# Optimization experiments

Measured on AMD Instinct MI355X. Metric: run time of the kernel, lower is better.

Reference implementation:

```python
import jax, jax.numpy as jnp
import numpy as np

N = 50000      # nodes
E = 800000     # edges (self-loop-free; reference appends self loops like PyG GATv2Conv)
IN = 128; H = 4; C = 64; HC = H * C; HID = 64; OUT = 2


def _gat_conv(x, wl, bl, wr, br, att, bias, src, dst, n):
    # PyG GATv2Conv: e_ij = att . leaky_relu(W_l x_j + W_r x_i); segment softmax over dst;
    # out_i = sum_j alpha_ij * (W_l x_j), heads concatenated, plus bias.
    xl = (x @ wl + bl).reshape(n, H, C)
    xr = (x @ wr + br).reshape(n, H, C)
    e = jnp.sum(att * jax.nn.leaky_relu(xl[src] + xr[dst], 0.2), axis=-1)  # [E+n, H]
    m = jax.ops.segment_max(e, dst, num_segments=n)                         # [n, H]
    ex = jnp.exp(e - m[dst])
    s = jax.ops.segment_sum(ex, dst, num_segments=n)
    alpha = ex / (s[dst] + 1e-16)
    out = jax.ops.segment_sum(xl[src] * alpha[..., None], dst, num_segments=n)
    return out.reshape(n, HC) + bias


def _graph_norm(x, w, b, ms, eps=1e-5):
    # PyG GraphNorm, single graph: normalize over all nodes
    mean = jnp.mean(x, axis=0)
    xc = x - ms * mean
    var = jnp.mean(xc * xc, axis=0)
    return w * xc / jnp.sqrt(var + eps) + b


def setup_inputs() -> dict:
    key = jax.random.key(0)
    k = jax.random.split(key, 16)
    x = jax.random.normal(k[0], (N, IN), dtype=jnp.float32)
    src = jax.random.randint(k[1], (E,), 0, N, dtype=jnp.int32)
    dst = jax.random.randint(k[2], (E,), 0, N, dtype=jnp.int32)
    dst = jnp.where(dst == src, (dst + 1) % N, dst)  # no self loops in raw edges
    edge_index = jnp.stack([src, dst])

    def lin(kk, fi, fo):
        return (jax.random.normal(kk, (fi, fo), jnp.float32) / np.float32(np.sqrt(fi)))

    zeros = lambda d: jnp.zeros((d,), jnp.float32)
    ones = lambda d: jnp.ones((d,), jnp.float32)
    return dict(
        x=x, edge_index=edge_index,
        conv0_wl=lin(k[3], IN, HC), conv0_bl=zeros(HC),
        conv0_wr=lin(k[4], IN, HC), conv0_br=zeros(HC),
        conv0_att=jax.random.normal(k[5], (H, C), jnp.float32) / np.float32(np.sqrt(C)),
        conv0_bias=zeros(HC),
        conv1_wl=lin(k[6], HC, HC), conv1_bl=zeros(HC),
        conv1_wr=lin(k[7], HC, HC), conv1_br=zeros(HC),
        conv1_att=jax.random.normal(k[8], (H, C), jnp.float32) / np.float32(np.sqrt(C)),
        conv1_bias=zeros(HC),
        gn0_w=ones(HC), gn0_b=zeros(HC), gn0_ms=ones(HC),
        gn1_w=ones(HC), gn1_b=zeros(HC), gn1_ms=ones(HC),
        lin0_w=lin(k[9], HC, HID), lin0_b=zeros(HID),
        lin1_w=lin(k[10], HID, HID), lin1_b=zeros(HID),
        lin2_w=lin(k[11], HID, OUT), lin2_b=zeros(OUT),
    )


def reference(x, edge_index, conv0_wl, conv0_bl, conv0_wr, conv0_br, conv0_att, conv0_bias,
              conv1_wl, conv1_bl, conv1_wr, conv1_br, conv1_att, conv1_bias,
              gn0_w, gn0_b, gn0_ms, gn1_w, gn1_b, gn1_ms,
              lin0_w, lin0_b, lin1_w, lin1_b, lin2_w, lin2_b):
    n = x.shape[0]
    loop = jnp.arange(n, dtype=edge_index.dtype)
    src = jnp.concatenate([edge_index[0], loop])  # add self loops (PyG default)
    dst = jnp.concatenate([edge_index[1], loop])
    # NOTE: original forward zips convs (3) with norms (2) -> only 2 convs execute.
    h = _gat_conv(x, conv0_wl, conv0_bl, conv0_wr, conv0_br, conv0_att, conv0_bias, src, dst, n)
    h = jax.nn.relu(_graph_norm(h, gn0_w, gn0_b, gn0_ms))
    h = _gat_conv(h, conv1_wl, conv1_bl, conv1_wr, conv1_br, conv1_att, conv1_bias, src, dst, n)
    h = jax.nn.relu(_graph_norm(h, gn1_w, gn1_b, gn1_ms))
    h = jax.nn.relu(h @ lin0_w + lin0_b)  # dropout_rate=None -> no dropout
    h = jax.nn.relu(h @ lin1_w + lin1_b)
    return h @ lin2_w + lin2_b
```

## Files before the change

kernel.cpp:

```cpp
#include <hip/hip_runtime.h>
#include <hip/hip_bf16.h>


typedef __bf16 bf16x8 __attribute__((ext_vector_type(8)));
typedef float  f32x4  __attribute__((ext_vector_type(4)));

__device__ __forceinline__ unsigned short f2b(float f) {
    unsigned u = __float_as_uint(f);
    return (unsigned short)((u + 0x7fffu + ((u >> 16) & 1u)) >> 16);
}

__device__ __forceinline__ unsigned pk_norm(unsigned u, float a0, float a1,
                                            float c0, float c1) {
    float lo = __uint_as_float(u << 16);
    float hi = __uint_as_float(u & 0xffff0000u);
    lo = fmaxf(fmaf(a0, lo, c0), 0.f);
    hi = fmaxf(fmaf(a1, hi, c1), 0.f);
    unsigned r;
    asm volatile("v_cvt_pk_bf16_f32 %0, %1, %2" : "=v"(r) : "v"(lo), "v"(hi));
    return r;
}

__device__ __forceinline__ void gload_lds16(const unsigned short* g, unsigned short* l) {
    __builtin_amdgcn_global_load_lds(
        (const __attribute__((address_space(1))) unsigned int*)g,
        (__attribute__((address_space(3))) unsigned int*)l, 16, 0, 0);
}

__global__ __launch_bounds__(256) void prep_all(
    const float* __restrict__ x, unsigned short* __restrict__ xbf, int nx4,
    const float* __restrict__ w0l, const float* __restrict__ w0r, unsigned short* __restrict__ Wt0,
    const float* __restrict__ w1l, const float* __restrict__ w1r, unsigned short* __restrict__ Wt1,
    const float* __restrict__ l0, unsigned short* __restrict__ Lt0,
    const float* __restrict__ l1, unsigned short* __restrict__ Lt1,
    float* __restrict__ zf, int* __restrict__ hist, int nh)
{
    int t = blockIdx.x * 256 + threadIdx.x;
    if (t < 512) { zf[t] = 0.f; }
    int i = t - 512;
    if (i >= 0 && i < nh) hist[i] = 0;
    i -= nh;
    if (i >= 0 && i < nx4) {
        float4 v = ((const float4*)x)[i];
        ushort4 o = { f2b(v.x), f2b(v.y), f2b(v.z), f2b(v.w) };
        ((ushort4*)xbf)[i] = o;
    }
    i -= nx4;
    if (i >= 0 && i < 32768) { int nn = i >> 7, kk = i & 127; Wt0[i] = f2b(w0l[kk * 256 + nn]); }
    i -= 32768;
    if (i >= 0 && i < 32768) { int nn = i >> 7, kk = i & 127; Wt0[32768 + i] = f2b(w0r[kk * 256 + nn]); }
    i -= 32768;
    if (i >= 0 && i < 65536) { int nn = i >> 8, kk = i & 255; Wt1[i] = f2b(w1l[kk * 256 + nn]); }
    i -= 65536;
    if (i >= 0 && i < 65536) { int nn = i >> 8, kk = i & 255; Wt1[65536 + i] = f2b(w1r[kk * 256 + nn]); }
    i -= 65536;
    if (i >= 0 && i < 16384) { int nn = i >> 8, kk = i & 255; Lt0[i] = f2b(l0[kk * 64 + nn]); }
    i -= 16384;
    if (i >= 0 && i < 4096)  { int nn = i >> 6, kk = i & 63;  Lt1[i] = f2b(l1[kk * 64 + nn]); }
}

template<int K, bool NORM>
__global__ __launch_bounds__(256) void conv_gemm(
    const unsigned short* __restrict__ A, const unsigned short* __restrict__ Bt,
    const float* __restrict__ bias0, const float* __restrict__ bias1, int split,
    const float* __restrict__ na, const float* __restrict__ nc,
    unsigned short* __restrict__ C, int M, int N, int nt)
{
    __shared__ unsigned short smem[128 * 136];
    unsigned short* sA = smem;
    unsigned short* sB = smem + 4096;

    const int nwg = gridDim.x;
    const int bid = blockIdx.x;
    const int q = nwg >> 3, r = nwg & 7;
    const int xcd = bid & 7, pos = bid >> 3;
    const int wgid = (xcd < r ? xcd * (q + 1) : r * (q + 1) + (xcd - r) * q) + pos;
    const int tm = wgid / nt;
    const int tn = wgid - tm * nt;

    const int lane = threadIdx.x & 63;
    const int w = threadIdx.x >> 6;
    const int wm = w >> 1, wn = w & 1;
    const int bm = tm * 128;
    const int bn = tn * 128;
    const int lr = lane & 15;
    const int g  = lane >> 4;

    const int srow = lane >> 2;
    const int sk   = ((lane & 3) ^ (srow & 3)) << 3;
    const int aslot = (g ^ (lr & 3)) << 3;

    f32x4 acc[4][4] = {};

    for (int k0 = 0; k0 < K; k0 += 32) {
        #pragma unroll
        for (int j = 0; j < 2; ++j) {
            const int row = w * 32 + j * 16 + srow;
            int ga = bm + row; if (ga >= M) ga = M - 1;
            gload_lds16(A + (size_t)ga * K + k0 + sk, sA + (size_t)(w * 32 + j * 16) * 32);
            gload_lds16(Bt + (size_t)(bn + row) * K + k0 + sk, sB + (size_t)(w * 32 + j * 16) * 32);
        }
        __syncthreads();

        bf16x8 afr[4], bfr[4];
        #pragma unroll
        for (int mi = 0; mi < 4; ++mi) {
            const int row = wm * 64 + mi * 16 + lr;
            afr[mi] = *(const bf16x8*)(sA + row * 32 + aslot);
        }
        #pragma unroll
        for (int ni = 0; ni < 4; ++ni) {
            const int row = wn * 64 + ni * 16 + lr;
            bfr[ni] = *(const bf16x8*)(sB + row * 32 + aslot);
        }
        if constexpr (NORM) {
            const int lk = g * 8;
            const float4 av0 = *(const float4*)(na + k0 + lk);
            const float4 av1 = *(const float4*)(na + k0 + lk + 4);
            const float4 cv0 = *(const float4*)(nc + k0 + lk);
            const float4 cv1 = *(const float4*)(nc + k0 + lk + 4);
            #pragma unroll
            for (int mi = 0; mi < 4; ++mi) {
                uint4 u = __builtin_bit_cast(uint4, afr[mi]);
                uint4 rr;
                rr.x = pk_norm(u.x, av0.x, av0.y, cv0.x, cv0.y);
                rr.y = pk_norm(u.y, av0.z, av0.w, cv0.z, cv0.w);
                rr.z = pk_norm(u.z, av1.x, av1.y, cv1.x, cv1.y);
                rr.w = pk_norm(u.w, av1.z, av1.w, cv1.z, cv1.w);
                afr[mi] = __builtin_bit_cast(bf16x8, rr);
            }
        }
        #pragma unroll
        for (int mi = 0; mi < 4; ++mi)
            #pragma unroll
            for (int ni = 0; ni < 4; ++ni)
                acc[mi][ni] = __builtin_amdgcn_mfma_f32_16x16x32_bf16(
                    bfr[ni], afr[mi], acc[mi][ni], 0, 0, 0);
        __syncthreads();
    }

    unsigned short (*cs)[136] = (unsigned short(*)[136])smem;
    #pragma unroll
    for (int ni = 0; ni < 4; ++ni) {
        const int lcol = wn * 64 + ni * 16 + g * 4;
        const int col = bn + lcol;
        const float4 bv = (col < split)
            ? *(const float4*)(bias0 + col)
            : *(const float4*)(bias1 + (col - split));
        #pragma unroll
        for (int mi = 0; mi < 4; ++mi) {
            const int lrow = wm * 64 + mi * 16 + lr;
            ushort4 o = { f2b(acc[mi][ni][0] + bv.x), f2b(acc[mi][ni][1] + bv.y),
                          f2b(acc[mi][ni][2] + bv.z), f2b(acc[mi][ni][3] + bv.w) };
            *(ushort4*)&cs[lrow][lcol] = o;
        }
    }
    __syncthreads();
    const int seg = threadIdx.x & 15;
    const int rb  = threadIdx.x >> 4;
    #pragma unroll
    for (int p = 0; p < 8; ++p) {
        const int lrow = p * 16 + rb;
        const int grow = bm + lrow;
        if (grow < M)
            *(uint4*)(C + (size_t)grow * N + bn + seg * 8) =
                *(const uint4*)&cs[lrow][seg * 8];
    }
}

template<int K, bool RELU, bool NORM>
__global__ __launch_bounds__(256) void mfma_gemm(
    const unsigned short* __restrict__ A, const unsigned short* __restrict__ Bt,
    const float* __restrict__ bias0, const float* __restrict__ bias1, int split,
    const float* __restrict__ na, const float* __restrict__ nc,
    unsigned short* __restrict__ C, int M, int N, int nt)
{
    __shared__ unsigned short cs[256][72];

    const int nwg = gridDim.x;
    const int bid = blockIdx.x;
    const int q = nwg >> 3, r = nwg & 7;
    const int xcd = bid & 7, pos = bid >> 3;
    const int wgid = (xcd < r ? xcd * (q + 1) : r * (q + 1) + (xcd - r) * q) + pos;
    const int tm = wgid / nt;
    const int tn = wgid - tm * nt;

    const int lane = threadIdx.x & 63;
    const int w = threadIdx.x >> 6;
    const int bm = tm * 256 + w * 64;
    const int bn = tn * 64;
    const int lr = lane & 15;
    const int g  = lane >> 4;
    const int lk = g * 8;

    f32x4 acc[4][4] = {};
    const unsigned short* pa[4];
    #pragma unroll
    for (int mi = 0; mi < 4; ++mi) {
        int rr = bm + mi * 16 + lr;
        if (rr >= M) rr = M - 1;
        pa[mi] = A + (size_t)rr * K + lk;
    }
    const unsigned short* pb = Bt + (size_t)(bn + lr) * K + lk;

    #pragma unroll
    for (int k0 = 0; k0 < K; k0 += 32) {
        bf16x8 bfr[4], afr[4];
        #pragma unroll
        for (int ni = 0; ni < 4; ++ni)
            bfr[ni] = *(const bf16x8*)(pb + (size_t)ni * 16 * K + k0);
        if constexpr (NORM) {
            const float4 av0 = *(const float4*)(na + k0 + lk);
            const float4 av1 = *(const float4*)(na + k0 + lk + 4);
            const float4 cv0 = *(const float4*)(nc + k0 + lk);
            const float4 cv1 = *(const float4*)(nc + k0 + lk + 4);
            #pragma unroll
            for (int mi = 0; mi < 4; ++mi) {
                uint4 u = *(const uint4*)(pa[mi] + k0);
                uint4 rr;
                rr.x = pk_norm(u.x, av0.x, av0.y, cv0.x, cv0.y);
                rr.y = pk_norm(u.y, av0.z, av0.w, cv0.z, cv0.w);
                rr.z = pk_norm(u.z, av1.x, av1.y, cv1.x, cv1.y);
                rr.w = pk_norm(u.w, av1.z, av1.w, cv1.z, cv1.w);
                afr[mi] = __builtin_bit_cast(bf16x8, rr);
            }
        } else {
            #pragma unroll
            for (int mi = 0; mi < 4; ++mi)
                afr[mi] = *(const bf16x8*)(pa[mi] + k0);
        }
        #pragma unroll
        for (int mi = 0; mi < 4; ++mi)
            #pragma unroll
            for (int ni = 0; ni < 4; ++ni)
                acc[mi][ni] = __builtin_amdgcn_mfma_f32_16x16x32_bf16(
                    bfr[ni], afr[mi], acc[mi][ni], 0, 0, 0);
    }

    #pragma unroll
    for (int ni = 0; ni < 4; ++ni) {
        const int colbase = bn + ni * 16 + g * 4;
        const float4 bv = (colbase < split)
            ? *(const float4*)(bias0 + colbase)
            : *(const float4*)(bias1 + (colbase - split));
        #pragma unroll
        for (int mi = 0; mi < 4; ++mi) {
            float v0 = acc[mi][ni][0] + bv.x;
            float v1 = acc[mi][ni][1] + bv.y;
            float v2 = acc[mi][ni][2] + bv.z;
            float v3 = acc[mi][ni][3] + bv.w;
            if (RELU) {
                v0 = fmaxf(v0, 0.f); v1 = fmaxf(v1, 0.f);
                v2 = fmaxf(v2, 0.f); v3 = fmaxf(v3, 0.f);
            }
            ushort4 o = { f2b(v0), f2b(v1), f2b(v2), f2b(v3) };
            *(ushort4*)&cs[w * 64 + mi * 16 + lr][ni * 16 + g * 4] = o;
        }
    }
    __syncthreads();
    const int row32 = threadIdx.x >> 3;
    const int seg = threadIdx.x & 7;
    #pragma unroll
    for (int p = 0; p < 8; ++p) {
        const int lrow = p * 32 + row32;
        const int grow = tm * 256 + lrow;
        if (grow < M)
            *(uint4*)(C + (size_t)grow * N + bn + seg * 8) =
                *(const uint4*)&cs[lrow][seg * 8];
    }
}

__global__ void hist_kernel(const int* __restrict__ dst, int E, int* __restrict__ hist) {
    int e = blockIdx.x * 256 + threadIdx.x;
    if (e < E) atomicAdd(&hist[dst[e]], 1);
}
__global__ void blk_sum_kernel(const int* __restrict__ hist, int n, int* __restrict__ bsum) {
    __shared__ int lds[256];
    int t = threadIdx.x;
    int i = blockIdx.x * 256 + t;
    lds[t] = (i < n) ? hist[i] : 0;
    __syncthreads();
    for (int off = 128; off > 0; off >>= 1) {
        if (t < off) lds[t] += lds[t + off];
        __syncthreads();
    }
    if (t == 0) bsum[blockIdx.x] = lds[0];
}
__global__ void bsum_scan_kernel(int* __restrict__ bsum, int nblk,
                                 int* __restrict__ row_ptr, int n) {
    __shared__ int lds[256];
    int t = threadIdx.x;
    int v = (t < nblk) ? bsum[t] : 0;
    lds[t] = v;
    __syncthreads();
    for (int off = 1; off < 256; off <<= 1) {
        int u = (t >= off) ? lds[t - off] : 0;
        __syncthreads();
        lds[t] += u;
        __syncthreads();
    }
    if (t < nblk) bsum[t] = lds[t] - v;
    if (t == 255) row_ptr[n] = lds[255];
}
__global__ void final_scan_kernel(const int* __restrict__ hist, const int* __restrict__ bsum,
                                  int n, int* __restrict__ row_ptr, int* __restrict__ cursor) {
    __shared__ int lds[256];
    int t = threadIdx.x;
    int i = blockIdx.x * 256 + t;
    int v = (i < n) ? hist[i] : 0;
    lds[t] = v;
    __syncthreads();
    for (int off = 1; off < 256; off <<= 1) {
        int u = (t >= off) ? lds[t - off] : 0;
        __syncthreads();
        lds[t] += u;
        __syncthreads();
    }
    if (i < n) {
        int ex = bsum[blockIdx.x] + lds[t] - v;
        row_ptr[i] = ex;
        cursor[i] = ex;
    }
}
__global__ void scatter_kernel(const int* __restrict__ src, const int* __restrict__ dst,
                               int E, int* cursor, int* __restrict__ esrc)
{
    int e = blockIdx.x * 256 + threadIdx.x;
    if (e < E) {
        int pos = atomicAdd(&cursor[dst[e]], 1);
        esrc[pos] = src[e];
    }
}

template<int CTRL>
__device__ __forceinline__ float dppadd(float v) {
    return v + __int_as_float(__builtin_amdgcn_update_dpp(
        0, __float_as_int(v), CTRL, 0xf, 0xf, true));
}
__device__ __forceinline__ float red8(float v) {
    v = dppadd<0xB1>(v);
    v = dppadd<0x4E>(v);
    v = dppadd<0x141>(v);
    return v;
}
__device__ __forceinline__ f32x4 unpA(uint4 u) {
    f32x4 r;
    r.x = __uint_as_float(u.x << 16); r.y = __uint_as_float(u.y << 16);
    r.z = __uint_as_float(u.z << 16); r.w = __uint_as_float(u.w << 16);
    return r;
}
__device__ __forceinline__ f32x4 unpB(uint4 u) {
    f32x4 r;
    r.x = __uint_as_float(u.x & 0xffff0000u); r.y = __uint_as_float(u.y & 0xffff0000u);
    r.z = __uint_as_float(u.z & 0xffff0000u); r.w = __uint_as_float(u.w & 0xffff0000u);
    return r;
}

__global__ __launch_bounds__(256) void gat_aggregate(
    const unsigned short* __restrict__ xlr, const float* __restrict__ att,
    const int* __restrict__ row_ptr, const int* __restrict__ esrc,
    const float* __restrict__ bias, unsigned short* __restrict__ out, int n)
{
    const int lane = threadIdx.x & 63;
    const int node = __builtin_amdgcn_readfirstlane(blockIdx.x * 4 + (threadIdx.x >> 6));
    if (node >= n) return;
    const int sub = lane & 31;
    const int half = lane >> 5;
    const int c8 = sub * 8;

    const float LOG2E = 1.4426950408889634f;
    const float4 a0 = *(const float4*)(att + c8);
    const float4 a1 = *(const float4*)(att + c8 + 4);
    f32x4 attA = { a0.x, a0.z, a1.x, a1.z };
    f32x4 attB = { a0.y, a0.w, a1.y, a1.w };
    attA *= LOG2E; attB *= LOG2E;

    const uint4 xru = *(const uint4*)(xlr + (size_t)node * 512 + 256 + c8);
    const f32x4 xrA = unpA(xru), xrB = unpB(xru);

    float m = -1e30f, s = 0.f;
    f32x4 accA = {}, accB = {};

    const int start = row_ptr[node];
    const int cnt = row_ptr[node + 1] - start + 1;
    const int kmax = (cnt + 1) >> 1;

    int idx = half;
    int srcv = (idx == 0) ? node : ((idx < cnt) ? esrc[start + idx - 1] : node);
    uint4 nu = *(const uint4*)(xlr + (size_t)srcv * 512 + c8);

    for (int k = 0; k < kmax; ++k) {
        const f32x4 vA = unpA(nu), vB = unpB(nu);
        const float mask = (idx < cnt) ? 1.f : 0.f;
        const int idxn = idx + 2;
        const int srcn = (idxn < cnt) ? esrc[start + idxn - 1] : node;
        nu = *(const uint4*)(xlr + (size_t)srcn * 512 + c8);

        const f32x4 zA = vA + xrA, zB = vB + xrB;
        const f32x4 tA = __builtin_elementwise_max(zA, zA * 0.2f);
        const f32x4 tB = __builtin_elementwise_max(zB, zB * 0.2f);
        f32x4 p = attA * tA;
        p = __builtin_elementwise_fma(attB, tB, p);
        const float e = red8((p.x + p.z) + (p.y + p.w));

        const float d = e - m;
        if (__builtin_expect(__any(d > 8.f), 0)) {
            const float mn = fmaxf(m, e);
            const float cs = __builtin_amdgcn_exp2f(m - mn);
            const float w  = __builtin_amdgcn_exp2f(e - mn) * mask;
            s = fmaf(s, cs, w);
            const f32x4 w4 = { w, w, w, w }, cv = { cs, cs, cs, cs };
            accA = __builtin_elementwise_fma(accA, cv, w4 * vA);
            accB = __builtin_elementwise_fma(accB, cv, w4 * vB);
            m = mn;
        } else {
            const float w = __builtin_amdgcn_exp2f(d) * mask;
            s += w;
            const f32x4 w4 = { w, w, w, w };
            accA = __builtin_elementwise_fma(w4, vA, accA);
            accB = __builtin_elementwise_fma(w4, vB, accB);
        }
        idx = idxn;
    }

    const float m_o = __shfl_xor(m, 32);
    const float s_o = __shfl_xor(s, 32);
    f32x4 accAo, accBo;
    accAo.x = __shfl_xor(accA.x, 32); accAo.y = __shfl_xor(accA.y, 32);
    accAo.z = __shfl_xor(accA.z, 32); accAo.w = __shfl_xor(accA.w, 32);
    accBo.x = __shfl_xor(accB.x, 32); accBo.y = __shfl_xor(accB.y, 32);
    accBo.z = __shfl_xor(accB.z, 32); accBo.w = __shfl_xor(accB.w, 32);
    const float mn = fmaxf(m, m_o);
    const float c0 = __builtin_amdgcn_exp2f(m - mn);
    const float c1 = __builtin_amdgcn_exp2f(m_o - mn);
    const float st = s * c0 + s_o * c1;
    const float inv = 1.f / (st + 1e-16f);

    if (half == 0) {
        const f32x4 oA = (accA * c0 + accAo * c1) * inv;
        const f32x4 oB = (accB * c0 + accBo * c1) * inv;
        const float4 b0 = *(const float4*)(bias + c8);
        const float4 b1 = *(const float4*)(bias + c8 + 4);
        uint4 o;
        o.x = (unsigned)f2b(oA.x + b0.x) | ((unsigned)f2b(oB.x + b0.y) << 16);
        o.y = (unsigned)f2b(oA.y + b0.z) | ((unsigned)f2b(oB.y + b0.w) << 16);
        o.z = (unsigned)f2b(oA.z + b1.x) | ((unsigned)f2b(oB.z + b1.y) << 16);
        o.w = (unsigned)f2b(oA.w + b1.z) | ((unsigned)f2b(oB.w + b1.w) << 16);
        *(uint4*)(out + (size_t)node * 256 + c8) = o;
    }
}

__global__ __launch_bounds__(256) void colstats_bf16(
    const unsigned short* __restrict__ x, int n,
    float* __restrict__ sum, float* __restrict__ sumsq)
{
    const int c = threadIdx.x;
    float s = 0.f, q = 0.f;
    for (int r = blockIdx.x; r < n; r += gridDim.x) {
        float v = __uint_as_float(((unsigned)x[(size_t)r * 256 + c]) << 16);
        s += v;
        q = fmaf(v, v, q);
    }
    atomicAdd(&sum[c], s);
    atomicAdd(&sumsq[c], q);
}
__global__ void norm_finalize(float* __restrict__ sum, float* __restrict__ sumsq,
                              const float* __restrict__ w, const float* __restrict__ b,
                              const float* __restrict__ ms,
                              float* __restrict__ a, float* __restrict__ c2, float invn)
{
    int i = threadIdx.x;
    float mean = sum[i] * invn;
    float ex2 = sumsq[i] * invn;
    float m = ms[i];
    float var = ex2 - 2.f * m * mean * mean + m * m * mean * mean;
    float av = w[i] * rsqrtf(var + 1e-5f);
    a[i] = av;
    c2[i] = b[i] - av * m * mean;
    sum[i] = 0.f;
    sumsq[i] = 0.f;
}

__global__ void lin2_kernel(const unsigned short* __restrict__ h, const float* __restrict__ w,
                            const float* __restrict__ b, float* __restrict__ out, int n)
{
    int i = blockIdx.x * 256 + threadIdx.x;
    if (i >= n) return;
    float a0 = b[0], a1 = b[1];
    const unsigned short* hr = h + (size_t)i * 64;
    #pragma unroll
    for (int k = 0; k < 64; ++k) {
        float v = __uint_as_float(((unsigned)hr[k]) << 16);
        a0 = fmaf(v, w[k * 2 + 0], a0);
        a1 = fmaf(v, w[k * 2 + 1], a1);
    }
    out[i * 2 + 0] = a0;
    out[i * 2 + 1] = a1;
}

extern "C" void kernel_launch(void* const* d_in, const int* in_sizes, int n_in,
                              void* d_out, int out_size, void* d_ws, size_t ws_size,
                              hipStream_t stream)
{
    const float* x      = (const float*)d_in[0];
    const int*   eidx   = (const int*)d_in[1];
    const float* c0_wl  = (const float*)d_in[2];
    const float* c0_bl  = (const float*)d_in[3];
    const float* c0_wr  = (const float*)d_in[4];
    const float* c0_br  = (const float*)d_in[5];
    const float* c0_att = (const float*)d_in[6];
    const float* c0_bias= (const float*)d_in[7];
    const float* c1_wl  = (const float*)d_in[8];
    const float* c1_bl  = (const float*)d_in[9];
    const float* c1_wr  = (const float*)d_in[10];
    const float* c1_br  = (const float*)d_in[11];
    const float* c1_att = (const float*)d_in[12];
    const float* c1_bias= (const float*)d_in[13];
    const float* gn0_w  = (const float*)d_in[14];
    const float* gn0_b  = (const float*)d_in[15];
    const float* gn0_ms = (const float*)d_in[16];
    const float* gn1_w  = (const float*)d_in[17];
    const float* gn1_b  = (const float*)d_in[18];
    const float* gn1_ms = (const float*)d_in[19];
    const float* lin0_w = (const float*)d_in[20];
    const float* lin0_b = (const float*)d_in[21];
    const float* lin1_w = (const float*)d_in[22];
    const float* lin1_b = (const float*)d_in[23];
    const float* lin2_w = (const float*)d_in[24];
    const float* lin2_b = (const float*)d_in[25];

    const int n = in_sizes[0] / 128;
    const int E = in_sizes[1] / 2;
    const int* src = eidx;
    const int* dst = eidx + E;

    char* wsp = (char*)d_ws;
    size_t off = 0;
    auto alloc = [&](size_t bytes) -> void* {
        void* p = wsp + off;
        off = (off + bytes + 255) & ~(size_t)255;
        return p;
    };
    unsigned short* xbf  = (unsigned short*)alloc((size_t)n * 128 * 2);
    unsigned short* xlr  = (unsigned short*)alloc((size_t)n * 512 * 2);
    unsigned short* hbB  = (unsigned short*)alloc((size_t)n * 256 * 2);
    unsigned short* mbuf = (unsigned short*)alloc((size_t)n * 64 * 2);
    unsigned short* mbuf2= (unsigned short*)alloc((size_t)n * 64 * 2);
    unsigned short* Wt0  = (unsigned short*)alloc((size_t)512 * 128 * 2);
    unsigned short* Wt1  = (unsigned short*)alloc((size_t)512 * 256 * 2);
    unsigned short* Lt0  = (unsigned short*)alloc((size_t)64 * 256 * 2);
    unsigned short* Lt1  = (unsigned short*)alloc((size_t)64 * 64 * 2);
    int*   esrc    = (int*)alloc((size_t)E * 4);
    int*   row_ptr = (int*)alloc((size_t)(n + 1) * 4);
    int*   cursor  = (int*)alloc((size_t)n * 4);
    int*   hist    = (int*)alloc((size_t)n * 4);
    int*   bsum    = (int*)alloc((size_t)256 * 4);
    float* s_sum   = (float*)alloc(256 * 4);
    float* s_sq    = (float*)alloc(256 * 4);
    float* s_a     = (float*)alloc(256 * 4);
    float* s_c     = (float*)alloc(256 * 4);

    const int nx4 = n * 128 / 4;
    const int prep_total = 512 + n + nx4 + 32768 * 2 + 65536 * 2 + 16384 + 4096;
    prep_all<<<(prep_total + 255) / 256, 256, 0, stream>>>(
        x, xbf, nx4, c0_wl, c0_wr, Wt0, c1_wl, c1_wr, Wt1,
        lin0_w, Lt0, lin1_w, Lt1, s_sum, hist, n);

    const int nblk = (n + 255) / 256;
    hist_kernel<<<(E + 255) / 256, 256, 0, stream>>>(dst, E, hist);
    blk_sum_kernel<<<nblk, 256, 0, stream>>>(hist, n, bsum);
    bsum_scan_kernel<<<1, 256, 0, stream>>>(bsum, nblk, row_ptr, n);
    final_scan_kernel<<<nblk, 256, 0, stream>>>(hist, bsum, n, row_ptr, cursor);
    scatter_kernel<<<(E + 255) / 256, 256, 0, stream>>>(src, dst, E, cursor, esrc);

    const int mtc = (n + 127) / 128;
    const int mt  = (n + 255) / 256;
    const int gagg = (n + 3) / 4;

    conv_gemm<128, false><<<mtc * 4, 256, 0, stream>>>(
        xbf, Wt0, c0_bl, c0_br, 256, nullptr, nullptr, xlr, n, 512, 4);
    gat_aggregate<<<gagg, 256, 0, stream>>>(xlr, c0_att, row_ptr, esrc, c0_bias, hbB, n);
    colstats_bf16<<<512, 256, 0, stream>>>(hbB, n, s_sum, s_sq);
    norm_finalize<<<1, 256, 0, stream>>>(s_sum, s_sq, gn0_w, gn0_b, gn0_ms, s_a, s_c, 1.f / n);

    conv_gemm<256, true><<<mtc * 4, 256, 0, stream>>>(
        hbB, Wt1, c1_bl, c1_br, 256, s_a, s_c, xlr, n, 512, 4);
    gat_aggregate<<<gagg, 256, 0, stream>>>(xlr, c1_att, row_ptr, esrc, c1_bias, hbB, n);
    colstats_bf16<<<512, 256, 0, stream>>>(hbB, n, s_sum, s_sq);
    norm_finalize<<<1, 256, 0, stream>>>(s_sum, s_sq, gn1_w, gn1_b, gn1_ms, s_a, s_c, 1.f / n);

    mfma_gemm<256, true, true><<<mt, 256, 0, stream>>>(
        hbB, Lt0, lin0_b, lin0_b, 64, s_a, s_c, mbuf, n, 64, 1);
    mfma_gemm<64, true, false><<<mt, 256, 0, stream>>>(
        mbuf, Lt1, lin1_b, lin1_b, 64, nullptr, nullptr, mbuf2, n, 64, 1);
    lin2_kernel<<<(n + 255) / 256, 256, 0, stream>>>(mbuf2, lin2_w, lin2_b, (float*)d_out, n);
}
```

Before: 386.8 us.

## Fuse MLP head into one kernel, merge scan kernels, widen colstats grid

Replaces the two MLP GEMM kernels and the final linear kernel with one fused kernel. Each wave keeps its 64-row intermediate activations in LDS instead of writing them to global memory and reading them back. The block-sum scan is folded into the final scan kernel, with each block redundantly scanning the block sums, which removes one launch. The column-statistics grid is doubled. In exchange, hidden activations are still rounded to bf16 between layers, and the lin2 step does a per-lane scalar dot product from LDS.

```diff
diff --git a/kernel.cpp b/kernel.cpp
--- a/kernel.cpp
+++ b/kernel.cpp
@@ -168,27 +168,28 @@
     }
 }
 
-template<int K, bool RELU, bool NORM>
-__global__ __launch_bounds__(256) void mfma_gemm(
-    const unsigned short* __restrict__ A, const unsigned short* __restrict__ Bt,
-    const float* __restrict__ bias0, const float* __restrict__ bias1, int split,
+__global__ __launch_bounds__(256) void mlp_fused(
+    const unsigned short* __restrict__ A,
+    const unsigned short* __restrict__ L0t,
+    const float* __restrict__ b0,
     const float* __restrict__ na, const float* __restrict__ nc,
-    unsigned short* __restrict__ C, int M, int N, int nt)
-{
-    __shared__ unsigned short cs[256][72];
+    const unsigned short* __restrict__ L1t,
+    const float* __restrict__ b1,
+    const float* __restrict__ w2,
+    const float* __restrict__ b2,
+    float* __restrict__ out, int M)
+{
+    __shared__ unsigned short hbuf[4][64][72];
 
     const int nwg = gridDim.x;
     const int bid = blockIdx.x;
     const int q = nwg >> 3, r = nwg & 7;
     const int xcd = bid & 7, pos = bid >> 3;
-    const int wgid = (xcd < r ? xcd * (q + 1) : r * (q + 1) + (xcd - r) * q) + pos;
-    const int tm = wgid / nt;
-    const int tn = wgid - tm * nt;
+    const int tm = (xcd < r ? xcd * (q + 1) : r * (q + 1) + (xcd - r) * q) + pos;
 
     const int lane = threadIdx.x & 63;
     const int w = threadIdx.x >> 6;
     const int bm = tm * 256 + w * 64;
-    const int bn = tn * 64;
     const int lr = lane & 15;
     const int g  = lane >> 4;
     const int lk = g * 8;
@@ -199,35 +200,27 @@
     for (int mi = 0; mi < 4; ++mi) {
         int rr = bm + mi * 16 + lr;
         if (rr >= M) rr = M - 1;
-        pa[mi] = A + (size_t)rr * K + lk;
-    }
-    const unsigned short* pb = Bt + (size_t)(bn + lr) * K + lk;
-
-    #pragma unroll
-    for (int k0 = 0; k0 < K; k0 += 32) {
+        pa[mi] = A + (size_t)rr * 256 + lk;
+    }
+    #pragma unroll
+    for (int k0 = 0; k0 < 256; k0 += 32) {
         bf16x8 bfr[4], afr[4];
         #pragma unroll
         for (int ni = 0; ni < 4; ++ni)
-            bfr[ni] = *(const bf16x8*)(pb + (size_t)ni * 16 * K + k0);
-        if constexpr (NORM) {
-            const float4 av0 = *(const float4*)(na + k0 + lk);
-            const float4 av1 = *(const float4*)(na + k0 + lk + 4);
-            const float4 cv0 = *(const float4*)(nc + k0 + lk);
-            const float4 cv1 = *(const float4*)(nc + k0 + lk + 4);
-            #pragma unroll
-            for (int mi = 0; mi < 4; ++mi) {
-                uint4 u = *(const uint4*)(pa[mi] + k0);
-                uint4 rr;
-                rr.x = pk_norm(u.x, av0.x, av0.y, cv0.x, cv0.y);
-                rr.y = pk_norm(u.y, av0.z, av0.w, cv0.z, cv0.w);
-                rr.z = pk_norm(u.z, av1.x, av1.y, cv1.x, cv1.y);
-                rr.w = pk_norm(u.w, av1.z, av1.w, cv1.z, cv1.w);
-                afr[mi] = __builtin_bit_cast(bf16x8, rr);
-            }
-        } else {
-            #pragma unroll
-            for (int mi = 0; mi < 4; ++mi)
-                afr[mi] = *(const bf16x8*)(pa[mi] + k0);
+            bfr[ni] = *(const bf16x8*)(L0t + (size_t)(ni * 16 + lr) * 256 + k0 + lk);
+        const float4 av0 = *(const float4*)(na + k0 + lk);
+        const float4 av1 = *(const float4*)(na + k0 + lk + 4);
+        const float4 cv0 = *(const float4*)(nc + k0 + lk);
+        const float4 cv1 = *(const float4*)(nc + k0 + lk + 4);
+        #pragma unroll
+        for (int mi = 0; mi < 4; ++mi) {
+            uint4 u = *(const uint4*)(pa[mi] + k0);
+            uint4 rr;
+            rr.x = pk_norm(u.x, av0.x, av0.y, cv0.x, cv0.y);
+            rr.y = pk_norm(u.y, av0.z, av0.w, cv0.z, cv0.w);
+            rr.z = pk_norm(u.z, av1.x, av1.y, cv1.x, cv1.y);
+            rr.w = pk_norm(u.w, av1.z, av1.w, cv1.z, cv1.w);
+            afr[mi] = __builtin_bit_cast(bf16x8, rr);
         }
         #pragma unroll
         for (int mi = 0; mi < 4; ++mi)
@@ -236,37 +229,72 @@
                 acc[mi][ni] = __builtin_amdgcn_mfma_f32_16x16x32_bf16(
                     bfr[ni], afr[mi], acc[mi][ni], 0, 0, 0);
     }
-
     #pragma unroll
     for (int ni = 0; ni < 4; ++ni) {
-        const int colbase = bn + ni * 16 + g * 4;
-        const float4 bv = (colbase < split)
-            ? *(const float4*)(bias0 + colbase)
-            : *(const float4*)(bias1 + (colbase - split));
+        const int col = ni * 16 + g * 4;
+        const float4 bv = *(const float4*)(b0 + col);
         #pragma unroll
         for (int mi = 0; mi < 4; ++mi) {
-            float v0 = acc[mi][ni][0] + bv.x;
-            float v1 = acc[mi][ni][1] + bv.y;
-            float v2 = acc[mi][ni][2] + bv.z;
-            float v3 = acc[mi][ni][3] + bv.w;
-            if (RELU) {
-                v0 = fmaxf(v0, 0.f); v1 = fmaxf(v1, 0.f);
-                v2 = fmaxf(v2, 0.f); v3 = fmaxf(v3, 0.f);
-            }
-            ushort4 o = { f2b(v0), f2b(v1), f2b(v2), f2b(v3) };
-            *(ushort4*)&cs[w * 64 + mi * 16 + lr][ni * 16 + g * 4] = o;
-        }
-    }
-    __syncthreads();
-    const int row32 = threadIdx.x >> 3;
-    const int seg = threadIdx.x & 7;
-    #pragma unroll
-    for (int p = 0; p < 8; ++p) {
-        const int lrow = p * 32 + row32;
-        const int grow = tm * 256 + lrow;
-        if (grow < M)
-            *(uint4*)(C + (size_t)grow * N + bn + seg * 8) =
-                *(const uint4*)&cs[lrow][seg * 8];
+            ushort4 o = { f2b(fmaxf(acc[mi][ni][0] + bv.x, 0.f)),
+                          f2b(fmaxf(acc[mi][ni][1] + bv.y, 0.f)),
+                          f2b(fmaxf(acc[mi][ni][2] + bv.z, 0.f)),
+                          f2b(fmaxf(acc[mi][ni][3] + bv.w, 0.f)) };
+            *(ushort4*)&hbuf[w][mi * 16 + lr][col] = o;
+        }
+    }
+
+    f32x4 acc2[4][4] = {};
+    #pragma unroll
+    for (int k0 = 0; k0 < 64; k0 += 32) {
+        bf16x8 bfr[4], afr[4];
+        #pragma unroll
+        for (int ni = 0; ni < 4; ++ni)
+            bfr[ni] = *(const bf16x8*)(L1t + (size_t)(ni * 16 + lr) * 64 + k0 + lk);
+        #pragma unroll
+        for (int mi = 0; mi < 4; ++mi)
+            afr[mi] = *(const bf16x8*)&hbuf[w][mi * 16 + lr][k0 + lk];
+        #pragma unroll
+        for (int mi = 0; mi < 4; ++mi)
+            #pragma unroll
+            for (int ni = 0; ni < 4; ++ni)
+                acc2[mi][ni] = __builtin_amdgcn_mfma_f32_16x16x32_bf16(
+                    bfr[ni], afr[mi], acc2[mi][ni], 0, 0, 0);
+    }
+    #pragma unroll
+    for (int ni = 0; ni < 4; ++ni) {
+        const int col = ni * 16 + g * 4;
+        const float4 bv = *(const float4*)(b1 + col);
+        #pragma unroll
+        for (int mi = 0; mi < 4; ++mi) {
+            ushort4 o = { f2b(fmaxf(acc2[mi][ni][0] + bv.x, 0.f)),
+                          f2b(fmaxf(acc2[mi][ni][1] + bv.y, 0.f)),
+                          f2b(fmaxf(acc2[mi][ni][2] + bv.z, 0.f)),
+                          f2b(fmaxf(acc2[mi][ni][3] + bv.w, 0.f)) };
+            *(ushort4*)&hbuf[w][mi * 16 + lr][col] = o;
+        }
+    }
+
+    float o0 = b2[0], o1 = b2[1];
+    #pragma unroll
+    for (int kb = 0; kb < 8; ++kb) {
+        bf16x8 hv = *(const bf16x8*)&hbuf[w][lane][kb * 8];
+        uint4 u = __builtin_bit_cast(uint4, hv);
+        const unsigned uu[4] = { u.x, u.y, u.z, u.w };
+        #pragma unroll
+        for (int j = 0; j < 4; ++j) {
+            const int k = kb * 8 + j * 2;
+            float lo = __uint_as_float(uu[j] << 16);
+            float hi = __uint_as_float(uu[j] & 0xffff0000u);
+            o0 = fmaf(lo, w2[k * 2 + 0], o0);
+            o1 = fmaf(lo, w2[k * 2 + 1], o1);
+            o0 = fmaf(hi, w2[k * 2 + 2], o0);
+            o1 = fmaf(hi, w2[k * 2 + 3], o1);
+        }
+    }
+    const int grow = bm + lane;
+    if (grow < M) {
+        out[grow * 2 + 0] = o0;
+        out[grow * 2 + 1] = o1;
     }
 }
 
@@ -286,41 +314,32 @@
     }
     if (t == 0) bsum[blockIdx.x] = lds[0];
 }
-__global__ void bsum_scan_kernel(int* __restrict__ bsum, int nblk,
-                                 int* __restrict__ row_ptr, int n) {
+__global__ void final_scan_kernel(const int* __restrict__ hist, const int* __restrict__ bsum,
+                                  int nblk, int n, int* __restrict__ row_ptr,
+                                  int* __restrict__ cursor) {
     __shared__ int lds[256];
+    __shared__ int boff[256];
     int t = threadIdx.x;
-    int v = (t < nblk) ? bsum[t] : 0;
-    lds[t] = v;
-    __syncthreads();
-    for (int off = 1; off < 256; off <<= 1) {
-        int u = (t >= off) ? lds[t - off] : 0;
-        __syncthreads();
-        lds[t] += u;
-        __syncthreads();
-    }
-    if (t < nblk) bsum[t] = lds[t] - v;
-    if (t == 255) row_ptr[n] = lds[255];
-}
-__global__ void final_scan_kernel(const int* __restrict__ hist, const int* __restrict__ bsum,
-                                  int n, int* __restrict__ row_ptr, int* __restrict__ cursor) {
-    __shared__ int lds[256];
-    int t = threadIdx.x;
+    boff[t] = (t < nblk) ? bsum[t] : 0;
     int i = blockIdx.x * 256 + t;
     int v = (i < n) ? hist[i] : 0;
     lds[t] = v;
     __syncthreads();
     for (int off = 1; off < 256; off <<= 1) {
-        int u = (t >= off) ? lds[t - off] : 0;
+        int u  = (t >= off) ? lds[t - off] : 0;
+        int u2 = (t >= off) ? boff[t - off] : 0;
         __syncthreads();
         lds[t] += u;
+        boff[t] += u2;
         __syncthreads();
     }
     if (i < n) {
-        int ex = bsum[blockIdx.x] + lds[t] - v;
+        int base = (blockIdx.x == 0) ? 0 : boff[blockIdx.x - 1];
+        int ex = base + lds[t] - v;
         row_ptr[i] = ex;
         cursor[i] = ex;
     }
+    if (blockIdx.x == 0 && t == 0) row_ptr[n] = boff[nblk - 1];
 }
 __global__ void scatter_kernel(const int* __restrict__ src, const int* __restrict__ dst,
                                int E, int* cursor, int* __restrict__ esrc)
@@ -479,23 +498,6 @@
     c2[i] = b[i] - av * m * mean;
     sum[i] = 0.f;
     sumsq[i] = 0.f;
-}
-
-__global__ void lin2_kernel(const unsigned short* __restrict__ h, const float* __restrict__ w,
-                            const float* __restrict__ b, float* __restrict__ out, int n)
-{
-    int i = blockIdx.x * 256 + threadIdx.x;
-    if (i >= n) return;
-    float a0 = b[0], a1 = b[1];
-    const unsigned short* hr = h + (size_t)i * 64;
-    #pragma unroll
-    for (int k = 0; k < 64; ++k) {
-        float v = __uint_as_float(((unsigned)hr[k]) << 16);
-        a0 = fmaf(v, w[k * 2 + 0], a0);
-        a1 = fmaf(v, w[k * 2 + 1], a1);
-    }
-    out[i * 2 + 0] = a0;
-    out[i * 2 + 1] = a1;
 }
 
 extern "C" void kernel_launch(void* const* d_in, const int* in_sizes, int n_in,
@@ -544,8 +546,6 @@
     unsigned short* xbf  = (unsigned short*)alloc((size_t)n * 128 * 2);
     unsigned short* xlr  = (unsigned short*)alloc((size_t)n * 512 * 2);
     unsigned short* hbB  = (unsigned short*)alloc((size_t)n * 256 * 2);
-    unsigned short* mbuf = (unsigned short*)alloc((size_t)n * 64 * 2);
-    unsigned short* mbuf2= (unsigned short*)alloc((size_t)n * 64 * 2);
     unsigned short* Wt0  = (unsigned short*)alloc((size_t)512 * 128 * 2);
     unsigned short* Wt1  = (unsigned short*)alloc((size_t)512 * 256 * 2);
     unsigned short* Lt0  = (unsigned short*)alloc((size_t)64 * 256 * 2);
@@ -569,8 +569,7 @@
     const int nblk = (n + 255) / 256;
     hist_kernel<<<(E + 255) / 256, 256, 0, stream>>>(dst, E, hist);
     blk_sum_kernel<<<nblk, 256, 0, stream>>>(hist, n, bsum);
-    bsum_scan_kernel<<<1, 256, 0, stream>>>(bsum, nblk, row_ptr, n);
-    final_scan_kernel<<<nblk, 256, 0, stream>>>(hist, bsum, n, row_ptr, cursor);
+    final_scan_kernel<<<nblk, 256, 0, stream>>>(hist, bsum, nblk, n, row_ptr, cursor);
     scatter_kernel<<<(E + 255) / 256, 256, 0, stream>>>(src, dst, E, cursor, esrc);
 
     const int mtc = (n + 127) / 128;
@@ -580,18 +579,15 @@
     conv_gemm<128, false><<<mtc * 4, 256, 0, stream>>>(
         xbf, Wt0, c0_bl, c0_br, 256, nullptr, nullptr, xlr, n, 512, 4);
     gat_aggregate<<<gagg, 256, 0, stream>>>(xlr, c0_att, row_ptr, esrc, c0_bias, hbB, n);
-    colstats_bf16<<<512, 256, 0, stream>>>(hbB, n, s_sum, s_sq);
+    colstats_bf16<<<1024, 256, 0, stream>>>(hbB, n, s_sum, s_sq);
     norm_finalize<<<1, 256, 0, stream>>>(s_sum, s_sq, gn0_w, gn0_b, gn0_ms, s_a, s_c, 1.f / n);
 
     conv_gemm<256, true><<<mtc * 4, 256, 0, stream>>>(
         hbB, Wt1, c1_bl, c1_br, 256, s_a, s_c, xlr, n, 512, 4);
     gat_aggregate<<<gagg, 256, 0, stream>>>(xlr, c1_att, row_ptr, esrc, c1_bias, hbB, n);
-    colstats_bf16<<<512, 256, 0, stream>>>(hbB, n, s_sum, s_sq);
+    colstats_bf16<<<1024, 256, 0, stream>>>(hbB, n, s_sum, s_sq);
     norm_finalize<<<1, 256, 0, stream>>>(s_sum, s_sq, gn1_w, gn1_b, gn1_ms, s_a, s_c, 1.f / n);
 
-    mfma_gemm<256, true, true><<<mt, 256, 0, stream>>>(
-        hbB, Lt0, lin0_b, lin0_b, 64, s_a, s_c, mbuf, n, 64, 1);
-    mfma_gemm<64, true, false><<<mt, 256, 0, stream>>>(
-        mbuf, Lt1, lin1_b, lin1_b, 64, nullptr, nullptr, mbuf2, n, 64, 1);
-    lin2_kernel<<<(n + 255) / 256, 256, 0, stream>>>(mbuf2, lin2_w, lin2_b, (float*)d_out, n);
-}
+    mlp_fused<<<mt, 256, 0, stream>>>(
+        hbB, Lt0, lin0_b, s_a, s_c, Lt1, lin1_b, lin2_w, lin2_b, (float*)d_out, n);
+}
```

Result: no change. 384.9 us (-0.5%).
